# Kernel tuning notes

Hardware: AMD Instinct MI355X
Metric: run time of the kernel (lower is better)

Reference implementation:

```python
import jax, jax.numpy as jnp
import numpy as np

B, S, QD, KD = 8, 8192, 1024, 1024
AD = min(QD, KD)
EPS = 1e-5


def _ste(x, xq):
    # straight-through estimator: forward uses xq, gradient flows as identity
    return x + jax.lax.stop_gradient(xq - x)


def bitlinear(x, w, b):
    """BitNet b1.58-style BitLinear: ternary per-tensor weight quant,
    per-token int8 absmax activation quant, both with STE."""
    s = jnp.mean(jnp.abs(w)) + EPS                      # per-tensor weight scale
    wq = _ste(w, jnp.clip(jnp.round(w / s), -1.0, 1.0) * s)
    g = jnp.max(jnp.abs(x), axis=-1, keepdims=True) + EPS  # per-token act scale
    xq = _ste(x, jnp.clip(jnp.round(x * (127.0 / g)), -128.0, 127.0) * (g / 127.0))
    return jnp.matmul(xq, wq.T) + b


def setup_inputs() -> dict:
    key = jax.random.key(0)
    ks = jax.random.split(key, 6)
    sc = 0.02
    return {
        "query": jax.random.normal(ks[0], (B, QD), dtype=jnp.float32),
        "context_memory": jax.random.normal(ks[1], (B, S, KD), dtype=jnp.float32),
        "w_q": jax.random.normal(ks[2], (AD, QD), dtype=jnp.float32) * sc,
        "b_q": jnp.zeros((AD,), dtype=jnp.float32),
        "w_k": jax.random.normal(ks[3], (AD, KD), dtype=jnp.float32) * sc,
        "b_k": jnp.zeros((AD,), dtype=jnp.float32),
        "w_v": jax.random.normal(ks[4], (QD, KD), dtype=jnp.float32) * sc,
        "b_v": jnp.zeros((QD,), dtype=jnp.float32),
        "w_c": jax.random.normal(ks[5], (QD, 2 * QD), dtype=jnp.float32) * sc,
        "b_c": jnp.zeros((QD,), dtype=jnp.float32),
    }


def reference(query, context_memory, w_q, b_q, w_k, b_k, w_v, b_v, w_c, b_c):
    attention_dim = w_q.shape[0]
    q = bitlinear(query, w_q, b_q)                 # [B, A]
    k = bitlinear(context_memory, w_k, b_k)        # [B, S, A]
    v = bitlinear(context_memory, w_v, b_v)        # [B, S, QD]
    scores = jnp.einsum('ba,bsa->bs', q, k) / (attention_dim ** 0.5)
    attn = jax.nn.softmax(scores, axis=-1)         # [B, S]
    ctx = jnp.einsum('bs,bsq->bq', attn, v)        # [B, QD]
    combined = jnp.concatenate([query, ctx], axis=-1)  # [B, 2*QD]
    return bitlinear(combined, w_c, b_c)           # [B, QD]
```

## Files before the change

### kernel.cpp

```cpp
#include <hip/hip_runtime.h>
#include <hip/hip_bf16.h>
#include <math.h>

#define EPS 1e-5f

static constexpr int Bb = 8;
static constexpr int Ss = 8192;
static constexpr int Dd = 1024;
static constexpr int NW = 128;
static constexpr int NWv = NW * 4;
static constexpr int TOK = Ss / NWv;
static constexpr int NCH = 64;
static constexpr int RC = Dd / NCH;


__device__ __forceinline__ float blk_reduce(float v, bool ismax, volatile float* lds) {
#pragma unroll
  for (int msk = 32; msk; msk >>= 1) {
    float o = __shfl_xor(v, msk);
    v = ismax ? fmaxf(v, o) : (v + o);
  }
  int w = threadIdx.x >> 6;
  __syncthreads();
  if ((threadIdx.x & 63) == 0) lds[w] = v;
  __syncthreads();
  return ismax ? fmaxf(fmaxf(lds[0], lds[1]), fmaxf(lds[2], lds[3]))
               : (lds[0] + lds[1] + lds[2] + lds[3]);
}

__device__ __forceinline__ float wred_max(float v) {
#pragma unroll
  for (int msk = 32; msk; msk >>= 1) v = fmaxf(v, __shfl_xor(v, msk));
  return v;
}

__device__ __forceinline__ float wred_sum(float v) {
#pragma unroll
  for (int msk = 32; msk; msk >>= 1) v += __shfl_xor(v, msk);
  return v;
}

__device__ __forceinline__ float quantf(float x, float c) {
  return fminf(fmaxf(rintf(x * c), -128.f), 127.f);
}

__device__ __forceinline__ float ternf(float w, float s) {
  return fminf(fmaxf(rintf(w / s), -1.f), 1.f);
}

__device__ __forceinline__ float4 tern4(float4 w, float s) {
  return make_float4(ternf(w.x, s), ternf(w.y, s), ternf(w.z, s), ternf(w.w, s));
}

__device__ __forceinline__ float4 quant4(float4 v, float c) {
  return make_float4(quantf(v.x, c), quantf(v.y, c), quantf(v.z, c), quantf(v.w, c));
}

__device__ __forceinline__ float absmax4(float4 v) {
  return fmaxf(fmaxf(fabsf(v.x), fabsf(v.y)), fmaxf(fabsf(v.z), fabsf(v.w)));
}


__global__ __launch_bounds__(256) void k_scales(
    const float* __restrict__ w0, const float* __restrict__ w1,
    const float* __restrict__ w2, const float* __restrict__ w3,
    double* __restrict__ part, float* __restrict__ scales, int* __restrict__ cnt)
{
  int seg = blockIdx.x >> 6;
  int blk = blockIdx.x & 63;
  const float* w = seg == 0 ? w0 : seg == 1 ? w1 : seg == 2 ? w2 : w3;
  int n4 = (seg == 3 ? (1024 * 2048) : (1024 * 1024)) >> 2;
  const float4* w4 = (const float4*)w;
  double acc = 0.0;
  for (int i = blk * 256 + threadIdx.x; i < n4; i += 64 * 256) {
    float4 v = w4[i];
    acc += (double)fabsf(v.x) + (double)fabsf(v.y)
         + (double)fabsf(v.z) + (double)fabsf(v.w);
  }
  __shared__ double sred[256];
  sred[threadIdx.x] = acc;
  __syncthreads();
  for (int s = 128; s > 0; s >>= 1) {
    if (threadIdx.x < s) sred[threadIdx.x] += sred[threadIdx.x + s];
    __syncthreads();
  }
  __shared__ int lastold;
  if (threadIdx.x == 0) {
    part[blockIdx.x] = sred[0];
    __threadfence();
    lastold = atomicAdd(cnt, 1);
  }
  __syncthreads();
  if (lastold == 255) {
    __threadfence();
    if (threadIdx.x < 4) {
      int sg = threadIdx.x;
      double s = 0.0;
      for (int i = 0; i < 64; i++) s += part[sg * 64 + i];
      double n = (sg == 3) ? 2097152.0 : 1048576.0;
      scales[sg] = (float)(s / n) + EPS;
    }
  }
}


__global__ __launch_bounds__(256) void k_qgemv(
    const float* __restrict__ query, const float* __restrict__ W,
    const float* __restrict__ bias, const float* __restrict__ scales,
    float* __restrict__ out)
{
  __shared__ float cs[Dd];
  __shared__ float red[4];
  int b = blockIdx.x >> 8, grp = blockIdx.x & 255;
  int tid = threadIdx.x, wv = tid >> 6, lane = tid & 63;
  float4 v = ((const float4*)(query + (size_t)b * Dd))[tid];
  float am = blk_reduce(absmax4(v), true, red);
  float g = am + EPS;
  float c = 127.0f / g;
  ((float4*)cs)[tid] = quant4(v, c);
  __syncthreads();
  float s = scales[0];
  int o = grp * 4 + wv;
  const float4* wr = (const float4*)(W + (size_t)o * Dd);
  float acc = 0.f;
#pragma unroll
  for (int i = 0; i < 4; i++) {
    int idx = i * 64 + lane;
    float4 w4 = wr[idx];
    float4 a4 = ((const float4*)cs)[idx];
    acc += a4.x * ternf(w4.x, s) + a4.y * ternf(w4.y, s)
         + a4.z * ternf(w4.z, s) + a4.w * ternf(w4.w, s);
  }
  acc = wred_sum(acc);
  if (lane == 0) out[(size_t)b * Dd + o] = s * (g / 127.0f) * acc + bias[o];
}


__global__ __launch_bounds__(256) void k_qk(
    const float* __restrict__ q, const float* __restrict__ Wk,
    const float* __restrict__ bk, const float* __restrict__ scales,
    float* __restrict__ part, float* __restrict__ qk, float* __restrict__ qdotbk,
    int* __restrict__ cnt)
{
  __shared__ float qs[Bb * RC];
  int ch = blockIdx.x;
  int a0 = ch * RC;
  int tid = threadIdx.x;
  if (tid < Bb * RC) {
    int b = tid / RC, a = tid - b * RC;
    qs[tid] = q[(size_t)b * Dd + a0 + a];
  }
  __syncthreads();
  float s = scales[1];
  float4 acc[Bb];
#pragma unroll
  for (int b = 0; b < Bb; b++) acc[b] = make_float4(0.f, 0.f, 0.f, 0.f);
  const float4* Wr = (const float4*)(Wk + (size_t)a0 * Dd);
  for (int i = 0; i < RC; i++) {
    float4 t4 = tern4(Wr[(size_t)i * 256 + tid], s);
#pragma unroll
    for (int b = 0; b < Bb; b++) {
      float qb = qs[b * RC + i];
      acc[b].x += qb * t4.x; acc[b].y += qb * t4.y;
      acc[b].z += qb * t4.z; acc[b].w += qb * t4.w;
    }
  }
#pragma unroll
  for (int b = 0; b < Bb; b++)
    ((float4*)part)[((size_t)ch * Bb + b) * 256 + tid] = acc[b];

  __threadfence();
  if (tid == 0) {
    atomicAdd(cnt, 1);
    while (__hip_atomic_load(cnt, __ATOMIC_ACQUIRE, __HIP_MEMORY_SCOPE_AGENT) < NCH)
      __builtin_amdgcn_s_sleep(8);
  }
  __syncthreads();
  __threadfence();

  int b = blockIdx.x >> 3, dc = blockIdx.x & 7;
  if (tid < 32) {
    int d4 = dc * 32 + tid;
    float4 a = make_float4(0.f, 0.f, 0.f, 0.f);
    for (int k = 0; k < NCH; k++) {
      float4 p = ((const float4*)part)[((size_t)k * Bb + b) * 256 + d4];
      a.x += p.x; a.y += p.y; a.z += p.z; a.w += p.w;
    }
    ((float4*)qk)[(size_t)b * 256 + d4] = make_float4(s * a.x, s * a.y, s * a.z, s * a.w);
  } else if (dc == 0 && tid >= 64 && tid < 128) {
    int lane = tid - 64;
    float p = 0.f;
    for (int a2 = lane; a2 < Dd; a2 += 64) p += q[(size_t)b * Dd + a2] * bk[a2];
    p = wred_sum(p);
    if (lane == 0) qdotbk[b] = p;
  }
}


__global__ __launch_bounds__(256, 4) void k_pass(
    const float* __restrict__ X, const float* __restrict__ qk,
    const float* __restrict__ qdotbk,
    float* __restrict__ m_part, float* __restrict__ l_part,
    float* __restrict__ t_part)
{
  int b    = blockIdx.x >> 7;
  int wg   = blockIdx.x & 127;
  int wv   = threadIdx.x >> 6;
  int lane = threadIdx.x & 63;
  int widx = wg * 4 + wv;
  int s0   = widx * TOK;

  const float4* qkb = (const float4*)(qk + (size_t)b * Dd);
  float4 qv0 = qkb[lane], qv1 = qkb[64 + lane], qv2 = qkb[128 + lane], qv3 = qkb[192 + lane];
  float qb = qdotbk[b];
  const float4* Xw = (const float4*)(X + ((size_t)b * Ss + s0) * Dd);

  float m = -INFINITY, l = 0.f;
  float4 a0 = make_float4(0,0,0,0), a1 = a0, a2 = a0, a3 = a0;

  for (int i = 0; i < TOK; i++) {
    size_t tb = (size_t)i * 256;
    float4 x0 = Xw[tb + lane],       x1 = Xw[tb + 64 + lane],
           x2 = Xw[tb + 128 + lane], x3 = Xw[tb + 192 + lane];

    float am = wred_max(fmaxf(fmaxf(absmax4(x0), absmax4(x1)),
                              fmaxf(absmax4(x2), absmax4(x3))));
    float g = am + EPS;
    float c = 127.0f / g;
    float gi = g / 127.0f;

    float q00 = rintf(x0.x * c), q01 = rintf(x0.y * c), q02 = rintf(x0.z * c), q03 = rintf(x0.w * c);
    float q10 = rintf(x1.x * c), q11 = rintf(x1.y * c), q12 = rintf(x1.z * c), q13 = rintf(x1.w * c);
    float q20 = rintf(x2.x * c), q21 = rintf(x2.y * c), q22 = rintf(x2.z * c), q23 = rintf(x2.w * c);
    float q30 = rintf(x3.x * c), q31 = rintf(x3.y * c), q32 = rintf(x3.z * c), q33 = rintf(x3.w * c);

    float dt = q00 * qv0.x + q01 * qv0.y + q02 * qv0.z + q03 * qv0.w
             + q10 * qv1.x + q11 * qv1.y + q12 * qv1.z + q13 * qv1.w
             + q20 * qv2.x + q21 * qv2.y + q22 * qv2.z + q23 * qv2.w
             + q30 * qv3.x + q31 * qv3.y + q32 * qv3.z + q33 * qv3.w;
    dt = wred_sum(dt);

    float score = (dt * gi + qb) * 0.03125f;
    if (score <= m) {
      float p  = __expf(score - m);
      l += p;
      float cf = p * gi;
      a0.x += cf * q00; a0.y += cf * q01; a0.z += cf * q02; a0.w += cf * q03;
      a1.x += cf * q10; a1.y += cf * q11; a1.z += cf * q12; a1.w += cf * q13;
      a2.x += cf * q20; a2.y += cf * q21; a2.z += cf * q22; a2.w += cf * q23;
      a3.x += cf * q30; a3.y += cf * q31; a3.z += cf * q32; a3.w += cf * q33;
    } else {
      float scl = __expf(m - score);
      l = l * scl + 1.0f;
      float cf = gi;
      a0.x = a0.x * scl + cf * q00; a0.y = a0.y * scl + cf * q01;
      a0.z = a0.z * scl + cf * q02; a0.w = a0.w * scl + cf * q03;
      a1.x = a1.x * scl + cf * q10; a1.y = a1.y * scl + cf * q11;
      a1.z = a1.z * scl + cf * q12; a1.w = a1.w * scl + cf * q13;
      a2.x = a2.x * scl + cf * q20; a2.y = a2.y * scl + cf * q21;
      a2.z = a2.z * scl + cf * q22; a2.w = a2.w * scl + cf * q23;
      a3.x = a3.x * scl + cf * q30; a3.y = a3.y * scl + cf * q31;
      a3.z = a3.z * scl + cf * q32; a3.w = a3.w * scl + cf * q33;
      m = score;
    }
  }

  size_t pidx = (size_t)b * NWv + widx;
  float4* tpw = (float4*)t_part + (size_t)pidx * 256;
  tpw[lane] = a0; tpw[64 + lane] = a1; tpw[128 + lane] = a2; tpw[192 + lane] = a3;
  if (lane == 0) { m_part[pidx] = m; l_part[pidx] = l; }
}


__global__ __launch_bounds__(256) void k_comb(
    const float* __restrict__ m_part, const float* __restrict__ l_part,
    const float* __restrict__ t_part, float* __restrict__ t16,
    float* __restrict__ t, int* __restrict__ cnt)
{
  __shared__ float red[4];
  int b = blockIdx.x >> 4, k = blockIdx.x & 15;
  int tid = threadIdx.x;
  float m1 = m_part[(size_t)b * NWv + tid];
  float m2 = m_part[(size_t)b * NWv + 256 + tid];
  float M = blk_reduce(fmaxf(m1, m2), true, red);
  float li = l_part[(size_t)b * NWv + tid] * __expf(m1 - M)
           + l_part[(size_t)b * NWv + 256 + tid] * __expf(m2 - M);
  float L = blk_reduce(li, false, red);

  float4 acc = make_float4(0,0,0,0);
  for (int i = 0; i < 32; i++) {
    size_t pi = (size_t)b * NWv + k * 32 + i;
    float w = __expf(m_part[pi] - M);
    float4 tp = ((const float4*)t_part)[pi * 256 + tid];
    acc.x += w * tp.x; acc.y += w * tp.y; acc.z += w * tp.z; acc.w += w * tp.w;
  }
  ((float4*)t16)[((size_t)(b * 16 + k)) * 256 + tid] = acc;

  __shared__ int lastold;
  if (tid == 0) {
    __threadfence();
    lastold = atomicAdd(&cnt[b], 1);
  }
  __syncthreads();
  if (lastold == 15) {
    __threadfence();
    float invL = 1.0f / L;
    float4 a = make_float4(0,0,0,0);
    for (int kk = 0; kk < 16; kk++) {
      float4 v = ((const float4*)t16)[((size_t)(b * 16 + kk)) * 256 + tid];
      a.x += v.x; a.y += v.y; a.z += v.z; a.w += v.w;
    }
    ((float4*)t)[(size_t)b * 256 + tid] =
        make_float4(a.x * invL, a.y * invL, a.z * invL, a.w * invL);
  }
}


__global__ __launch_bounds__(256) void k_tern_gemv_f32(
    const float* __restrict__ act, const float* __restrict__ W,
    const float* __restrict__ bias, const float* __restrict__ scales, int sidx,
    float* __restrict__ out, int K, int N)
{
  int wave = blockIdx.x * 4 + (threadIdx.x >> 6);
  int lane = threadIdx.x & 63;
  int b = wave / N, o = wave - b * N;
  float s = scales[sidx];
  const float4* wr = (const float4*)(W + (size_t)o * K);
  const float4* ar = (const float4*)(act + (size_t)b * K);
  int n4 = K >> 2;
  float acc = 0.f;
  for (int i = lane; i < n4; i += 64) {
    float4 w4 = wr[i];
    float4 a4 = ar[i];
    acc += a4.x * ternf(w4.x, s) + a4.y * ternf(w4.y, s)
         + a4.z * ternf(w4.z, s) + a4.w * ternf(w4.w, s);
  }
  acc = wred_sum(acc);
  if (lane == 0) out[(size_t)b * N + o] = s * acc + bias[o];
}


__global__ __launch_bounds__(256) void k_final(
    const float* __restrict__ query, const float* __restrict__ ctx,
    const float* __restrict__ W, const float* __restrict__ bias,
    const float* __restrict__ scales, float* __restrict__ out)
{
  __shared__ float cs[2 * Dd];
  __shared__ float red[4];
  int b = blockIdx.x >> 8, grp = blockIdx.x & 255;
  int tid = threadIdx.x, wv = tid >> 6, lane = tid & 63;
  float4 vq = ((const float4*)(query + (size_t)b * Dd))[tid];
  float4 vc = ((const float4*)(ctx   + (size_t)b * Dd))[tid];
  float am = blk_reduce(fmaxf(absmax4(vq), absmax4(vc)), true, red);
  float g = am + EPS;
  float c = 127.0f / g;
  ((float4*)cs)[tid]       = quant4(vq, c);
  ((float4*)cs)[256 + tid] = quant4(vc, c);
  __syncthreads();
  float s = scales[3];
  int o = grp * 4 + wv;
  const float4* wr = (const float4*)(W + (size_t)o * 2 * Dd);
  float acc = 0.f;
#pragma unroll
  for (int i = 0; i < 8; i++) {
    int idx = i * 64 + lane;
    float4 w4 = wr[idx];
    float4 a4 = ((const float4*)cs)[idx];
    acc += a4.x * ternf(w4.x, s) + a4.y * ternf(w4.y, s)
         + a4.z * ternf(w4.z, s) + a4.w * ternf(w4.w, s);
  }
  acc = wred_sum(acc);
  if (lane == 0) out[(size_t)b * Dd + o] = s * (g / 127.0f) * acc + bias[o];
}


extern "C" void kernel_launch(void* const* d_in, const int* in_sizes, int n_in,
                              void* d_out, int out_size, void* d_ws, size_t ws_size,
                              hipStream_t stream)
{
  const float* query = (const float*)d_in[0];
  const float* X     = (const float*)d_in[1];
  const float* w_q   = (const float*)d_in[2];
  const float* b_q   = (const float*)d_in[3];
  const float* w_k   = (const float*)d_in[4];
  const float* b_k   = (const float*)d_in[5];
  const float* w_v   = (const float*)d_in[6];
  const float* b_v   = (const float*)d_in[7];
  const float* w_c   = (const float*)d_in[8];
  const float* b_c   = (const float*)d_in[9];
  float* out = (float*)d_out;
  char* ws = (char*)d_ws;

  size_t off = 0;
  auto alloc = [&](size_t bytes) -> size_t {
    size_t o = off;
    off += (bytes + 255) & ~(size_t)255;
    return o;
  };
  size_t o_cnt    = alloc(256);
  size_t o_part   = alloc(256 * sizeof(double));
  size_t o_scales = alloc(4 * sizeof(float));
  size_t o_q      = alloc((size_t)Bb * Dd * 4);
  size_t o_qk     = alloc((size_t)Bb * Dd * 4);
  size_t o_qbk    = alloc(Bb * sizeof(float));
  size_t o_t      = alloc((size_t)Bb * Dd * 4);
  size_t o_ctx    = alloc((size_t)Bb * Dd * 4);
  size_t o_t16    = alloc((size_t)Bb * 16 * Dd * 4);
  size_t o_qkp    = alloc((size_t)NCH * Bb * Dd * 4);
  size_t o_mp     = alloc((size_t)Bb * NWv * 4);
  size_t o_lp     = alloc((size_t)Bb * NWv * 4);
  size_t o_tp     = alloc((size_t)Bb * NWv * Dd * 4);
  (void)ws_size;

  int*    cnt    = (int*)(ws + o_cnt);
  double* part   = (double*)(ws + o_part);
  float*  scales = (float*)(ws + o_scales);
  float*  qv     = (float*)(ws + o_q);
  float*  qk     = (float*)(ws + o_qk);
  float*  qbk    = (float*)(ws + o_qbk);
  float*  tvec   = (float*)(ws + o_t);
  float*  ctx    = (float*)(ws + o_ctx);
  float*  t16    = (float*)(ws + o_t16);
  float*  qkp    = (float*)(ws + o_qkp);
  float*  mp     = (float*)(ws + o_mp);
  float*  lp     = (float*)(ws + o_lp);
  float*  tp     = (float*)(ws + o_tp);

  hipMemsetAsync(ws + o_cnt, 0, 256, stream);
  k_scales<<<256, 256, 0, stream>>>(w_q, w_k, w_v, w_c, part, scales, &cnt[0]);
  k_qgemv<<<Bb * 256, 256, 0, stream>>>(query, w_q, b_q, scales, qv);
  k_qk<<<NCH, 256, 0, stream>>>(qv, w_k, b_k, scales, qkp, qk, qbk, &cnt[1]);
  k_pass<<<Bb * NW, 256, 0, stream>>>(X, qk, qbk, mp, lp, tp);
  k_comb<<<Bb * 16, 256, 0, stream>>>(mp, lp, tp, t16, tvec, &cnt[2]);
  k_tern_gemv_f32<<<(Bb * Dd) / 4, 256, 0, stream>>>(tvec, w_v, b_v, scales, 2, ctx, Dd, Dd);
  k_final<<<Bb * 256, 256, 0, stream>>>(query, ctx, w_c, b_c, scales, out);
}
```

Before: 142.8 us.

## Stream context tokens through LDS with async global-to-LDS prefetch and halve wave count

The pass kernel now prefetches each wave's next three tokens straight into LDS with global_load_lds into a four-slot ring buffer, waiting with s_waitcnt vmcnt before reading each token. This is meant to hide HBM latency that the direct per-iteration global loads exposed. The grid is halved (64 workgroups per batch, twice the tokens per wave), and the combine kernel shrinks its partial reduction to match. The 64KB of shared memory per block cuts occupancy, and the launch_bounds occupancy hint is dropped.

Measured after the change: 143.8 us. No clear change (+0.6%).

```diff
diff --git a/kernel.cpp b/kernel.cpp
--- a/kernel.cpp
+++ b/kernel.cpp
@@ -7,11 +7,14 @@
 static constexpr int Bb = 8;
 static constexpr int Ss = 8192;
 static constexpr int Dd = 1024;
-static constexpr int NW = 128;
+static constexpr int NW = 64;
 static constexpr int NWv = NW * 4;
 static constexpr int TOK = Ss / NWv;
 static constexpr int NCH = 64;
 static constexpr int RC = Dd / NCH;
+
+typedef const __attribute__((address_space(1))) void* gas_t;
+typedef __attribute__((address_space(3))) void* las_t;
 
 
 __device__ __forceinline__ float blk_reduce(float v, bool ismax, volatile float* lds) {
@@ -197,14 +200,26 @@
 }
 
 
-__global__ __launch_bounds__(256, 4) void k_pass(
+__device__ __forceinline__ void stage_tok(const float4* __restrict__ Xw,
+                                          float* dst, int tok, int lane) {
+#pragma unroll
+  for (int j = 0; j < 4; ++j) {
+    __builtin_amdgcn_global_load_lds(
+        (gas_t)(Xw + (size_t)tok * 256 + j * 64 + lane),
+        (las_t)(dst + j * 256),
+        16, 0, 0);
+  }
+}
+
+__global__ __launch_bounds__(256) void k_pass(
     const float* __restrict__ X, const float* __restrict__ qk,
     const float* __restrict__ qdotbk,
     float* __restrict__ m_part, float* __restrict__ l_part,
     float* __restrict__ t_part)
 {
-  int b    = blockIdx.x >> 7;
-  int wg   = blockIdx.x & 127;
+  __shared__ float sbuf[4][4][1024];
+  int b    = blockIdx.x >> 6;
+  int wg   = blockIdx.x & 63;
   int wv   = threadIdx.x >> 6;
   int lane = threadIdx.x & 63;
   int widx = wg * 4 + wv;
@@ -215,13 +230,18 @@
   float qb = qdotbk[b];
   const float4* Xw = (const float4*)(X + ((size_t)b * Ss + s0) * Dd);
 
+  stage_tok(Xw, sbuf[wv][0], 0, lane);
+  stage_tok(Xw, sbuf[wv][1], 1, lane);
+  stage_tok(Xw, sbuf[wv][2], 2, lane);
+
   float m = -INFINITY, l = 0.f;
   float4 a0 = make_float4(0,0,0,0), a1 = a0, a2 = a0, a3 = a0;
 
   for (int i = 0; i < TOK; i++) {
-    size_t tb = (size_t)i * 256;
-    float4 x0 = Xw[tb + lane],       x1 = Xw[tb + 64 + lane],
-           x2 = Xw[tb + 128 + lane], x3 = Xw[tb + 192 + lane];
+    asm volatile("s_waitcnt vmcnt(8)" ::: "memory");
+    __builtin_amdgcn_sched_barrier(0);
+    const float4* L = (const float4*)sbuf[wv][i & 3];
+    float4 x0 = L[lane], x1 = L[64 + lane], x2 = L[128 + lane], x3 = L[192 + lane];
 
     float am = wred_max(fmaxf(fmaxf(absmax4(x0), absmax4(x1)),
                               fmaxf(absmax4(x2), absmax4(x3))));
@@ -263,6 +283,8 @@
       a3.z = a3.z * scl + cf * q32; a3.w = a3.w * scl + cf * q33;
       m = score;
     }
+
+    if (i + 3 < TOK) stage_tok(Xw, sbuf[wv][(i + 3) & 3], i + 3, lane);
   }
 
   size_t pidx = (size_t)b * NWv + widx;
@@ -280,17 +302,15 @@
   __shared__ float red[4];
   int b = blockIdx.x >> 4, k = blockIdx.x & 15;
   int tid = threadIdx.x;
-  float m1 = m_part[(size_t)b * NWv + tid];
-  float m2 = m_part[(size_t)b * NWv + 256 + tid];
-  float M = blk_reduce(fmaxf(m1, m2), true, red);
-  float li = l_part[(size_t)b * NWv + tid] * __expf(m1 - M)
-           + l_part[(size_t)b * NWv + 256 + tid] * __expf(m2 - M);
+  float mi = m_part[(size_t)b * NWv + tid];
+  float M = blk_reduce(mi, true, red);
+  float li = l_part[(size_t)b * NWv + tid] * expf(mi - M);
   float L = blk_reduce(li, false, red);
 
   float4 acc = make_float4(0,0,0,0);
-  for (int i = 0; i < 32; i++) {
-    size_t pi = (size_t)b * NWv + k * 32 + i;
-    float w = __expf(m_part[pi] - M);
+  for (int i = 0; i < 16; i++) {
+    size_t pi = (size_t)b * NWv + k * 16 + i;
+    float w = expf(m_part[pi] - M);
     float4 tp = ((const float4*)t_part)[pi * 256 + tid];
     acc.x += w * tp.x; acc.y += w * tp.y; acc.z += w * tp.z; acc.w += w * tp.w;
   }
```
